# Kernel tuning notes

Hardware: AMD Instinct MI355X
Metric: run time of the kernel (lower is better)

## Reference

```python
import jax, jax.numpy as jnp
import numpy as np

N_HEADS, N_LEVELS, N_POINTS = 8, 4, 4
SPATIAL_SHAPES = np.array([[100, 100], [50, 50], [25, 25], [13, 13]], dtype=np.int32)


def setup_inputs() -> dict:
    key = jax.random.key(0)
    ks = jax.random.split(key, 6)
    N, Lq, C = 8, 4096, 256
    L_total = int(SPATIAL_SHAPES.prod(1).sum())  # 13294
    HLP = N_HEADS * N_LEVELS * N_POINTS  # 128
    return {
        "query": jax.random.normal(ks[0], (Lq, N, C), jnp.float32),
        "reference_points": jax.random.uniform(ks[1], (N, Lq, N_LEVELS, 2), jnp.float32),
        "feature_maps": jax.random.normal(ks[2], (L_total, N, C), jnp.float32),
        "spatial_shapes": SPATIAL_SHAPES,  # static numpy: drives reshapes
        "W_off": jax.random.normal(ks[3], (C, HLP * 2), jnp.float32) * 0.02,
        "b_off": jnp.zeros((HLP * 2,), jnp.float32),
        "W_attn": jax.random.normal(ks[4], (C, HLP), jnp.float32) * 0.02,
        "b_attn": jnp.zeros((HLP,), jnp.float32),
        "W_out": jax.random.normal(ks[5], (C, C), jnp.float32) / np.sqrt(C).astype(np.float32),
        "b_out": jnp.zeros((C,), jnp.float32),
    }


def bilinear_sample(img, gx, gy):
    """F.grid_sample(mode='bilinear', padding_mode='zeros', align_corners=False).
    img: (B, C, H, W); gx, gy: (B, P) normalized coords in [-1, 1]. -> (B, C, P)"""
    B, C, H, W = img.shape
    x = ((gx + 1.0) * W - 1.0) * 0.5
    y = ((gy + 1.0) * H - 1.0) * 0.5
    x0f = jnp.floor(x)
    y0f = jnp.floor(y)
    wx = x - x0f
    wy = y - y0f
    x0 = x0f.astype(jnp.int32)
    y0 = y0f.astype(jnp.int32)
    img_flat = img.reshape(B, C, H * W)

    def gather(ix, iy):
        valid = (ix >= 0) & (ix < W) & (iy >= 0) & (iy < H)
        idx = jnp.clip(iy, 0, H - 1) * W + jnp.clip(ix, 0, W - 1)  # (B, P)
        v = jax.vmap(lambda f, i: f[:, i])(img_flat, idx)  # (B, C, P)
        return v * valid[:, None, :].astype(img.dtype)

    v00 = gather(x0, y0)
    v01 = gather(x0 + 1, y0)
    v10 = gather(x0, y0 + 1)
    v11 = gather(x0 + 1, y0 + 1)
    w00 = ((1 - wx) * (1 - wy))[:, None, :]
    w01 = (wx * (1 - wy))[:, None, :]
    w10 = ((1 - wx) * wy)[:, None, :]
    w11 = (wx * wy)[:, None, :]
    return v00 * w00 + v01 * w01 + v10 * w10 + v11 * w11


def deform_attn(query, reference_points, feature_maps, spatial_shapes,
                W_off, b_off, W_attn, b_attn, W_out, b_out):
    Lq, N, C = query.shape
    H_, L_, P_ = N_HEADS, N_LEVELS, N_POINTS
    dh = C // H_
    q = jnp.transpose(query, (1, 0, 2))  # (N, Lq, C)
    off = (q @ W_off + b_off).reshape(N, Lq, H_, L_, P_, 2)
    attn = jax.nn.softmax((q @ W_attn + b_attn).reshape(N, Lq, H_, L_ * P_), axis=-1)
    attn = attn.reshape(N, Lq, H_, L_, P_)
    ss = np.asarray(spatial_shapes)  # (L, 2) as (H, W), static
    ss_flip = jnp.asarray(ss[:, ::-1].astype(np.float32))  # (L, 2) as (W, H)
    # sampling locations in [0,1], then to [-1,1] grid coords
    loc = reference_points[:, :, None, :, None, :] + off / ss_flip[None, None, None, :, None, :]
    grid = 2.0 * loc - 1.0  # (N, Lq, H, L, P, 2)
    starts = np.concatenate([[0], np.cumsum(ss.prod(1))[:-1]])
    sampled = []
    for lid in range(L_):
        Hl, Wl = int(ss[lid, 0]), int(ss[lid, 1])
        s = int(starts[lid])
        fm = feature_maps[s:s + Hl * Wl]  # (Hl*Wl, N, C)
        img = jnp.transpose(fm, (1, 2, 0)).reshape(N * H_, dh, Hl, Wl)
        g = jnp.transpose(grid[:, :, :, lid], (0, 2, 1, 3, 4)).reshape(N * H_, Lq * P_, 2)
        v = bilinear_sample(img, g[..., 0], g[..., 1])  # (N*H, dh, Lq*P)
        v = v.reshape(N, H_, dh, Lq, P_)
        sampled.append(jnp.transpose(v, (0, 3, 1, 2, 4)))  # (N, Lq, H, dh, P)
    sv = jnp.stack(sampled, axis=4)  # (N, Lq, H, dh, L, P)
    out = (attn[:, :, :, None, :, :] * sv).sum(axis=(-1, -2)).reshape(N, Lq, C)
    out = out @ W_out + b_out
    return jnp.transpose(out, (1, 0, 2))  # (Lq, N, C)


def reference(query, reference_points, feature_maps, spatial_shapes,
              W_off, b_off, W_attn, b_attn, W_out, b_out):
    return deform_attn(query, reference_points, feature_maps, spatial_shapes,
                       W_off, b_off, W_attn, b_attn, W_out, b_out)
```

## Files before the change

### kernel.cpp

```cpp
#include <hip/hip_runtime.h>

typedef unsigned short u16;
typedef __attribute__((ext_vector_type(8))) __bf16 bf16x8;
typedef __attribute__((ext_vector_type(4))) float f32x4;
typedef __attribute__((ext_vector_type(4))) int   i32x4;

#define NLQ 32768
#define WPN (384*256)
#define WON (256*256)
#define FMU 3403264

static __device__ __forceinline__ u16 f2bf(float f) {
    unsigned u = __float_as_uint(f);
    return (u16)((u + 0x7fffu + ((u >> 16) & 1u)) >> 16);
}
static __device__ __forceinline__ uint pk2(float lo, float hi) {
    return (uint)f2bf(lo) | ((uint)f2bf(hi) << 16);
}

__global__ __launch_bounds__(256) void wconv_kernel(
    const float* __restrict__ W_off, const float* __restrict__ W_attn,
    const float* __restrict__ W_out,
    u16* __restrict__ wtp, u16* __restrict__ wto)
{
    const int wi = blockIdx.x * 256 + threadIdx.x;
    if (wi < WPN) {
        int j = wi >> 8, k = wi & 255;
        float v = (j < 256) ? W_off[k * 256 + j] : W_attn[k * 128 + (j - 256)];
        wtp[wi] = f2bf(v);
    } else {
        int wi2 = wi - WPN;
        int j = wi2 >> 8, k = wi2 & 255;
        wto[wi2] = f2bf(W_out[k * 256 + j]);
    }
}

__global__ __launch_bounds__(256) void fmconv_kernel(
    const f32x4* __restrict__ fm, uint4* __restrict__ fmb)
{
    const int base = blockIdx.x * 2048 + threadIdx.x;
#pragma unroll
    for (int j = 0; j < 8; ++j) {
        int u = base + j * 256;
        if (u < FMU) {
            f32x4 lo = __builtin_nontemporal_load(fm + 2 * u);
            f32x4 hi = __builtin_nontemporal_load(fm + 2 * u + 1);
            uint4 r;
            r.x = pk2(lo.x, lo.y); r.y = pk2(lo.z, lo.w);
            r.z = pk2(hi.x, hi.y); r.w = pk2(hi.z, hi.w);
            fmb[u] = r;
        }
    }
}

__global__ __launch_bounds__(256) void proj_gemm(
    const float* __restrict__ query, const u16* __restrict__ Bt,
    const float* __restrict__ b_off, const float* __restrict__ b_attn,
    float* __restrict__ C)
{
    const int t = threadIdx.x;
    const int wid = t >> 6, lane = t & 63;
    const int lr = lane & 15, lk = lane >> 4;
    const int mrow = blockIdx.x * 128 + (wid >> 1) * 64;
    const int ncol = blockIdx.y * 128 + (wid & 1) * 64;
    const int kO = lk * 8;

    const float* qrow[4];
#pragma unroll
    for (int mi = 0; mi < 4; ++mi) {
        int gq = mrow + mi * 16 + lr;
        qrow[mi] = query + (size_t)((gq & 4095) * 8 + (gq >> 12)) * 256;
    }

    f32x4 acc[4][4] = {};
#pragma unroll
    for (int kk = 0; kk < 8; ++kk) {
        bf16x8 a[4], b[4];
#pragma unroll
        for (int mi = 0; mi < 4; ++mi) {
            f32x4 lo = *(const f32x4*)(qrow[mi] + kk * 32 + kO);
            f32x4 hi = *(const f32x4*)(qrow[mi] + kk * 32 + kO + 4);
#pragma unroll
            for (int j = 0; j < 4; ++j) {
                a[mi][j]     = (__bf16)lo[j];
                a[mi][4 + j] = (__bf16)hi[j];
            }
        }
#pragma unroll
        for (int ni = 0; ni < 4; ++ni)
            b[ni] = *(const bf16x8*)(Bt + (size_t)(ncol + ni * 16 + lr) * 256 + kk * 32 + kO);
#pragma unroll
        for (int mi = 0; mi < 4; ++mi)
#pragma unroll
            for (int ni = 0; ni < 4; ++ni)
                acc[mi][ni] = __builtin_amdgcn_mfma_f32_16x16x32_bf16(a[mi], b[ni], acc[mi][ni], 0, 0, 0);
    }

#pragma unroll
    for (int ni = 0; ni < 4; ++ni) {
        int gcol = ncol + ni * 16 + lr;
        float bias = (gcol < 256) ? b_off[gcol] : b_attn[gcol - 256];
#pragma unroll
        for (int mi = 0; mi < 4; ++mi) {
            f32x4 v = acc[mi][ni];
#pragma unroll
            for (int r = 0; r < 4; ++r)
                C[(size_t)(mrow + mi * 16 + lk * 4 + r) * 384 + gcol] = v[r] + bias;
        }
    }
}

__global__ __launch_bounds__(256) void sample_kernel(
    const u16* __restrict__ fmb,
    const float* __restrict__ proj,
    const float* __restrict__ refp,
    u16* __restrict__ mid)
{
    __shared__ i32x4 loff[256];
    __shared__ f32x4 lwv[256];
    const int t = threadIdx.x;
    const int ql = t >> 7, pt = t & 127;
    const int gq = blockIdx.x * 2 + ql;
    const int n = gq >> 12;

    {
        const int lp = pt & 15, l = lp >> 2;
        float lg = proj[(size_t)gq * 384 + 256 + pt];
        float m = lg;
#pragma unroll
        for (int msk = 1; msk < 16; msk <<= 1) m = fmaxf(m, __shfl_xor(m, msk));
        float e = __expf(lg - m);
        float s = e;
#pragma unroll
        for (int msk = 1; msk < 16; msk <<= 1) s += __shfl_xor(s, msk);
        float a = e / s;

        float ox = proj[(size_t)gq * 384 + 2 * pt];
        float oy = proj[(size_t)gq * 384 + 2 * pt + 1];
        int   Sl = (l == 0) ? 100 : (l == 1) ? 50 : (l == 2) ? 25 : 13;
        int   lb = (l == 0) ? 0 : (l == 1) ? 10000 : (l == 2) ? 12500 : 13125;
        float Sf = (float)Sl;
        float rx = refp[((size_t)gq * 4 + l) * 2 + 0];
        float ry = refp[((size_t)gq * 4 + l) * 2 + 1];
        float px = rx * Sf + ox - 0.5f;
        float py = ry * Sf + oy - 0.5f;
        float x0f = floorf(px), y0f = floorf(py);
        float wx = px - x0f, wy = py - y0f;
        int x0 = (int)x0f, y0 = (int)y0f;
        bool xv0 = (unsigned)x0 < (unsigned)Sl;
        bool xv1 = (unsigned)(x0 + 1) < (unsigned)Sl;
        bool yv0 = (unsigned)y0 < (unsigned)Sl;
        bool yv1 = (unsigned)(y0 + 1) < (unsigned)Sl;
        int x0c = min(max(x0, 0), Sl - 1), x1c = min(max(x0 + 1, 0), Sl - 1);
        int y0c = min(max(y0, 0), Sl - 1), y1c = min(max(y0 + 1, 0), Sl - 1);
        int r0 = (lb + y0c * Sl) << 12, r1 = (lb + y1c * Sl) << 12;
        i32x4 o; f32x4 w;
        o.x = r0 + (x0c << 12); o.y = r0 + (x1c << 12);
        o.z = r1 + (x0c << 12); o.w = r1 + (x1c << 12);
        w.x = (xv0 && yv0) ? a * (1.f - wx) * (1.f - wy) : 0.f;
        w.y = (xv1 && yv0) ? a * wx * (1.f - wy) : 0.f;
        w.z = (xv0 && yv1) ? a * (1.f - wx) * wy : 0.f;
        w.w = (xv1 && yv1) ? a * wx * wy : 0.f;
        loff[t] = o;
        lwv[t] = w;
    }
    __syncthreads();

    const int h = pt >> 4, ll = pt & 15, g2 = ll >> 2, cl = ll & 3;
    const uint boff = (uint)(n * 512 + h * 64 + cl * 16);
    const char* __restrict__ fb = (const char*)fmb;

    float a0 = 0.f, a1 = 0.f, a2 = 0.f, a3 = 0.f;
    float a4 = 0.f, a5 = 0.f, a6 = 0.f, a7 = 0.f;
#pragma unroll
    for (int pi = 0; pi < 4; ++pi) {
        int idx = ql * 128 + h * 16 + g2 * 4 + pi;
        i32x4 o = loff[idx];
        f32x4 w = lwv[idx];
        uint4 v0 = *(const uint4*)(fb + (boff + (uint)o.x));
        uint4 v1 = *(const uint4*)(fb + (boff + (uint)o.y));
        uint4 v2 = *(const uint4*)(fb + (boff + (uint)o.z));
        uint4 v3 = *(const uint4*)(fb + (boff + (uint)o.w));
#define ACC8(u, wt)                                        \
        a0 += wt * __uint_as_float(u.x << 16);             \
        a1 += wt * __uint_as_float(u.x & 0xFFFF0000u);     \
        a2 += wt * __uint_as_float(u.y << 16);             \
        a3 += wt * __uint_as_float(u.y & 0xFFFF0000u);     \
        a4 += wt * __uint_as_float(u.z << 16);             \
        a5 += wt * __uint_as_float(u.z & 0xFFFF0000u);     \
        a6 += wt * __uint_as_float(u.w << 16);             \
        a7 += wt * __uint_as_float(u.w & 0xFFFF0000u);
        ACC8(v0, w.x) ACC8(v1, w.y) ACC8(v2, w.z) ACC8(v3, w.w)
#undef ACC8
    }
#pragma unroll
    for (int msk = 4; msk <= 8; msk <<= 1) {
        a0 += __shfl_xor(a0, msk); a1 += __shfl_xor(a1, msk);
        a2 += __shfl_xor(a2, msk); a3 += __shfl_xor(a3, msk);
        a4 += __shfl_xor(a4, msk); a5 += __shfl_xor(a5, msk);
        a6 += __shfl_xor(a6, msk); a7 += __shfl_xor(a7, msk);
    }

    if (ll < 4) {
        uint4 r;
        r.x = pk2(a0, a1); r.y = pk2(a2, a3);
        r.z = pk2(a4, a5); r.w = pk2(a6, a7);
        ((uint4*)mid)[(size_t)gq * 32 + h * 4 + cl] = r;
    }
}

__global__ __launch_bounds__(256) void out_gemm(
    const u16* __restrict__ A, const u16* __restrict__ Bt,
    const float* __restrict__ b_out,
    float* __restrict__ out)
{
    const int t = threadIdx.x;
    const int wid = t >> 6, lane = t & 63;
    const int lr = lane & 15, lk = lane >> 4;
    const int mrow = blockIdx.x * 128 + (wid >> 1) * 64;
    const int ncol = blockIdx.y * 128 + (wid & 1) * 64;
    const int kO = lk * 8;

    f32x4 acc[4][4] = {};
#pragma unroll
    for (int kk = 0; kk < 8; ++kk) {
        bf16x8 a[4], b[4];
#pragma unroll
        for (int mi = 0; mi < 4; ++mi)
            a[mi] = *(const bf16x8*)(A + (size_t)(mrow + mi * 16 + lr) * 256 + kk * 32 + kO);
#pragma unroll
        for (int ni = 0; ni < 4; ++ni)
            b[ni] = *(const bf16x8*)(Bt + (size_t)(ncol + ni * 16 + lr) * 256 + kk * 32 + kO);
#pragma unroll
        for (int mi = 0; mi < 4; ++mi)
#pragma unroll
            for (int ni = 0; ni < 4; ++ni)
                acc[mi][ni] = __builtin_amdgcn_mfma_f32_16x16x32_bf16(a[mi], b[ni], acc[mi][ni], 0, 0, 0);
    }

#pragma unroll
    for (int ni = 0; ni < 4; ++ni) {
        int gcol = ncol + ni * 16 + lr;
        float bias = b_out[gcol];
#pragma unroll
        for (int mi = 0; mi < 4; ++mi) {
            f32x4 v = acc[mi][ni];
#pragma unroll
            for (int r = 0; r < 4; ++r) {
                int grow = mrow + mi * 16 + lk * 4 + r;
                int nn = grow >> 12, lq = grow & 4095;
                out[(size_t)(lq * 8 + nn) * 256 + gcol] = v[r] + bias;
            }
        }
    }
}

extern "C" void kernel_launch(void* const* d_in, const int* in_sizes, int n_in,
                              void* d_out, int out_size, void* d_ws, size_t ws_size,
                              hipStream_t stream) {
    const float* query  = (const float*)d_in[0];
    const float* refp   = (const float*)d_in[1];
    const float* fm     = (const float*)d_in[2];
    const float* W_off  = (const float*)d_in[4];
    const float* b_off  = (const float*)d_in[5];
    const float* W_attn = (const float*)d_in[6];
    const float* b_attn = (const float*)d_in[7];
    const float* W_out  = (const float*)d_in[8];
    const float* b_out  = (const float*)d_in[9];
    float* out = (float*)d_out;

    float* ws_proj = (float*)d_ws;
    u16*   wtp     = (u16*)(ws_proj + (size_t)NLQ * 384);
    u16*   wto     = wtp + (size_t)WPN;
    u16*   mid     = wto + (size_t)WON;
    u16*   fmb     = mid + (size_t)NLQ * 256;

    wconv_kernel<<<640, 256, 0, stream>>>(W_off, W_attn, W_out, wtp, wto);
    fmconv_kernel<<<1663, 256, 0, stream>>>((const f32x4*)fm, (uint4*)fmb);
    proj_gemm<<<dim3(256, 3), 256, 0, stream>>>(query, wtp, b_off, b_attn, ws_proj);
    sample_kernel<<<NLQ / 2, 256, 0, stream>>>(fmb, ws_proj, refp, mid);
    out_gemm<<<dim3(256, 2), 256, 0, stream>>>(mid, wto, b_out, out);
}
```

Before: 167.9 us.

## Switch pipeline to fp16, merge prep kernels, pre-convert query, use packed half FMA

```diff
diff --git a/kernel.cpp b/kernel.cpp
--- a/kernel.cpp
+++ b/kernel.cpp
@@ -1,7 +1,8 @@
 #include <hip/hip_runtime.h>
+#include <hip/hip_fp16.h>
 
 typedef unsigned short u16;
-typedef __attribute__((ext_vector_type(8))) __bf16 bf16x8;
+typedef __attribute__((ext_vector_type(8))) _Float16 f16x8;
 typedef __attribute__((ext_vector_type(4))) float f32x4;
 typedef __attribute__((ext_vector_type(4))) int   i32x4;
 
@@ -10,53 +11,78 @@
 #define WON (256*256)
 #define FMU 3403264
 
-static __device__ __forceinline__ u16 f2bf(float f) {
-    unsigned u = __float_as_uint(f);
-    return (u16)((u + 0x7fffu + ((u >> 16) & 1u)) >> 16);
-}
-static __device__ __forceinline__ uint pk2(float lo, float hi) {
-    return (uint)f2bf(lo) | ((uint)f2bf(hi) << 16);
-}
-
-__global__ __launch_bounds__(256) void wconv_kernel(
+static __device__ __forceinline__ uint pkh(float a, float b) {
+    __half2 h = __floats2half2_rn(a, b);
+    return *reinterpret_cast<uint*>(&h);
+}
+static __device__ __forceinline__ u16 f2h(float a) {
+    __half h = __float2half_rn(a);
+    return *reinterpret_cast<u16*>(&h);
+}
+static __device__ __forceinline__ __half2 bits2h2(uint u) {
+    return *reinterpret_cast<__half2*>(&u);
+}
+static __device__ __forceinline__ __half2 shfl_xor_h2(__half2 v, int m) {
+    int i = *reinterpret_cast<int*>(&v);
+    i = __shfl_xor(i, m);
+    return *reinterpret_cast<__half2*>(&i);
+}
+
+__global__ __launch_bounds__(256) void prep_kernel(
+    const f32x4* __restrict__ fm, uint4* __restrict__ fmb,
+    const float* __restrict__ query, uint4* __restrict__ qh4,
     const float* __restrict__ W_off, const float* __restrict__ W_attn,
     const float* __restrict__ W_out,
     u16* __restrict__ wtp, u16* __restrict__ wto)
 {
-    const int wi = blockIdx.x * 256 + threadIdx.x;
-    if (wi < WPN) {
-        int j = wi >> 8, k = wi & 255;
-        float v = (j < 256) ? W_off[k * 256 + j] : W_attn[k * 128 + (j - 256)];
-        wtp[wi] = f2bf(v);
+    const int b = blockIdx.x, t = threadIdx.x;
+    if (b < 1663) {
+        const int base = b * 2048 + t;
+#pragma unroll
+        for (int j = 0; j < 8; ++j) {
+            int u = base + j * 256;
+            if (u < FMU) {
+                f32x4 lo = __builtin_nontemporal_load(fm + 2 * u);
+                f32x4 hi = __builtin_nontemporal_load(fm + 2 * u + 1);
+                uint4 r;
+                r.x = pkh(lo.x, lo.y); r.y = pkh(lo.z, lo.w);
+                r.z = pkh(hi.x, hi.y); r.w = pkh(hi.z, hi.w);
+                fmb[u] = r;
+            }
+        }
+    } else if (b < 2175) {
+        const int base = (b - 1663) * 2048 + t;
+#pragma unroll
+        for (int j = 0; j < 8; ++j) {
+            int u = base + j * 256;
+            int gq = u >> 5, c = (u & 31) * 8;
+            int lq = gq & 4095, n = gq >> 12;
+            const f32x4* src = (const f32x4*)(query + ((size_t)(lq * 8 + n) << 8) + c);
+            f32x4 lo = __builtin_nontemporal_load(src);
+            f32x4 hi = __builtin_nontemporal_load(src + 1);
+            uint4 r;
+            r.x = pkh(lo.x, lo.y); r.y = pkh(lo.z, lo.w);
+            r.z = pkh(hi.x, hi.y); r.w = pkh(hi.z, hi.w);
+            qh4[u] = r;
+        }
     } else {
-        int wi2 = wi - WPN;
-        int j = wi2 >> 8, k = wi2 & 255;
-        wto[wi2] = f2bf(W_out[k * 256 + j]);
-    }
-}
-
-__global__ __launch_bounds__(256) void fmconv_kernel(
-    const f32x4* __restrict__ fm, uint4* __restrict__ fmb)
-{
-    const int base = blockIdx.x * 2048 + threadIdx.x;
-#pragma unroll
-    for (int j = 0; j < 8; ++j) {
-        int u = base + j * 256;
-        if (u < FMU) {
-            f32x4 lo = __builtin_nontemporal_load(fm + 2 * u);
-            f32x4 hi = __builtin_nontemporal_load(fm + 2 * u + 1);
-            uint4 r;
-            r.x = pk2(lo.x, lo.y); r.y = pk2(lo.z, lo.w);
-            r.z = pk2(hi.x, hi.y); r.w = pk2(hi.z, hi.w);
-            fmb[u] = r;
+        const int wi = (b - 2175) * 256 + t;
+        if (wi < WPN) {
+            int j = wi >> 8, k = wi & 255;
+            float v = (j < 256) ? W_off[k * 256 + j] : W_attn[k * 128 + (j - 256)];
+            wtp[wi] = f2h(v);
+        } else {
+            int wi2 = wi - WPN;
+            int j = wi2 >> 8, k = wi2 & 255;
+            wto[wi2] = f2h(W_out[k * 256 + j]);
         }
     }
 }
 
 __global__ __launch_bounds__(256) void proj_gemm(
-    const float* __restrict__ query, const u16* __restrict__ Bt,
+    const u16* __restrict__ A, const u16* __restrict__ Bt,
     const float* __restrict__ b_off, const float* __restrict__ b_attn,
-    float* __restrict__ C)
+    u16* __restrict__ C)
 {
     const int t = threadIdx.x;
     const int wid = t >> 6, lane = t & 63;
@@ -65,35 +91,21 @@
     const int ncol = blockIdx.y * 128 + (wid & 1) * 64;
     const int kO = lk * 8;
 
-    const float* qrow[4];
-#pragma unroll
-    for (int mi = 0; mi < 4; ++mi) {
-        int gq = mrow + mi * 16 + lr;
-        qrow[mi] = query + (size_t)((gq & 4095) * 8 + (gq >> 12)) * 256;
-    }
-
     f32x4 acc[4][4] = {};
 #pragma unroll
     for (int kk = 0; kk < 8; ++kk) {
-        bf16x8 a[4], b[4];
-#pragma unroll
-        for (int mi = 0; mi < 4; ++mi) {
-            f32x4 lo = *(const f32x4*)(qrow[mi] + kk * 32 + kO);
-            f32x4 hi = *(const f32x4*)(qrow[mi] + kk * 32 + kO + 4);
-#pragma unroll
-            for (int j = 0; j < 4; ++j) {
-                a[mi][j]     = (__bf16)lo[j];
-                a[mi][4 + j] = (__bf16)hi[j];
-            }
-        }
+        f16x8 a[4], b[4];
+#pragma unroll
+        for (int mi = 0; mi < 4; ++mi)
+            a[mi] = *(const f16x8*)(A + (size_t)(mrow + mi * 16 + lr) * 256 + kk * 32 + kO);
 #pragma unroll
         for (int ni = 0; ni < 4; ++ni)
-            b[ni] = *(const bf16x8*)(Bt + (size_t)(ncol + ni * 16 + lr) * 256 + kk * 32 + kO);
+            b[ni] = *(const f16x8*)(Bt + (size_t)(ncol + ni * 16 + lr) * 256 + kk * 32 + kO);
 #pragma unroll
         for (int mi = 0; mi < 4; ++mi)
 #pragma unroll
             for (int ni = 0; ni < 4; ++ni)
-                acc[mi][ni] = __builtin_amdgcn_mfma_f32_16x16x32_bf16(a[mi], b[ni], acc[mi][ni], 0, 0, 0);
+                acc[mi][ni] = __builtin_amdgcn_mfma_f32_16x16x32_f16(a[mi], b[ni], acc[mi][ni], 0, 0, 0);
     }
 
 #pragma unroll
@@ -105,19 +117,19 @@
             f32x4 v = acc[mi][ni];
 #pragma unroll
             for (int r = 0; r < 4; ++r)
-                C[(size_t)(mrow + mi * 16 + lk * 4 + r) * 384 + gcol] = v[r] + bias;
+                C[(size_t)(mrow + mi * 16 + lk * 4 + r) * 384 + gcol] = f2h(v[r] + bias);
         }
     }
 }
 
 __global__ __launch_bounds__(256) void sample_kernel(
     const u16* __restrict__ fmb,
-    const float* __restrict__ proj,
+    const u16* __restrict__ proj,
     const float* __restrict__ refp,
     u16* __restrict__ mid)
 {
     __shared__ i32x4 loff[256];
-    __shared__ f32x4 lwv[256];
+    __shared__ i32x4 lwp[256];
     const int t = threadIdx.x;
     const int ql = t >> 7, pt = t & 127;
     const int gq = blockIdx.x * 2 + ql;
@@ -125,7 +137,7 @@
 
     {
         const int lp = pt & 15, l = lp >> 2;
-        float lg = proj[(size_t)gq * 384 + 256 + pt];
+        float lg = __half2float(__ushort_as_half(proj[(size_t)gq * 384 + 256 + pt]));
         float m = lg;
 #pragma unroll
         for (int msk = 1; msk < 16; msk <<= 1) m = fmaxf(m, __shfl_xor(m, msk));
@@ -135,8 +147,8 @@
         for (int msk = 1; msk < 16; msk <<= 1) s += __shfl_xor(s, msk);
         float a = e / s;
 
-        float ox = proj[(size_t)gq * 384 + 2 * pt];
-        float oy = proj[(size_t)gq * 384 + 2 * pt + 1];
+        float ox = __half2float(__ushort_as_half(proj[(size_t)gq * 384 + 2 * pt]));
+        float oy = __half2float(__ushort_as_half(proj[(size_t)gq * 384 + 2 * pt + 1]));
         int   Sl = (l == 0) ? 100 : (l == 1) ? 50 : (l == 2) ? 25 : 13;
         int   lb = (l == 0) ? 0 : (l == 1) ? 10000 : (l == 2) ? 12500 : 13125;
         float Sf = (float)Sl;
@@ -154,15 +166,18 @@
         int x0c = min(max(x0, 0), Sl - 1), x1c = min(max(x0 + 1, 0), Sl - 1);
         int y0c = min(max(y0, 0), Sl - 1), y1c = min(max(y0 + 1, 0), Sl - 1);
         int r0 = (lb + y0c * Sl) << 12, r1 = (lb + y1c * Sl) << 12;
-        i32x4 o; f32x4 w;
+        i32x4 o;
         o.x = r0 + (x0c << 12); o.y = r0 + (x1c << 12);
         o.z = r1 + (x0c << 12); o.w = r1 + (x1c << 12);
-        w.x = (xv0 && yv0) ? a * (1.f - wx) * (1.f - wy) : 0.f;
-        w.y = (xv1 && yv0) ? a * wx * (1.f - wy) : 0.f;
-        w.z = (xv0 && yv1) ? a * (1.f - wx) * wy : 0.f;
-        w.w = (xv1 && yv1) ? a * wx * wy : 0.f;
+        float w0 = (xv0 && yv0) ? a * (1.f - wx) * (1.f - wy) : 0.f;
+        float w1 = (xv1 && yv0) ? a * wx * (1.f - wy) : 0.f;
+        float w2 = (xv0 && yv1) ? a * (1.f - wx) * wy : 0.f;
+        float w3 = (xv1 && yv1) ? a * wx * wy : 0.f;
+        i32x4 wp;
+        wp.x = (int)pkh(w0, w0); wp.y = (int)pkh(w1, w1);
+        wp.z = (int)pkh(w2, w2); wp.w = (int)pkh(w3, w3);
         loff[t] = o;
-        lwv[t] = w;
+        lwp[t] = wp;
     }
     __syncthreads();
 
@@ -170,41 +185,43 @@
     const uint boff = (uint)(n * 512 + h * 64 + cl * 16);
     const char* __restrict__ fb = (const char*)fmb;
 
-    float a0 = 0.f, a1 = 0.f, a2 = 0.f, a3 = 0.f;
-    float a4 = 0.f, a5 = 0.f, a6 = 0.f, a7 = 0.f;
+    __half2 z = __float2half2_rn(0.f);
+    __half2 a01 = z, a23 = z, a45 = z, a67 = z;
 #pragma unroll
     for (int pi = 0; pi < 4; ++pi) {
         int idx = ql * 128 + h * 16 + g2 * 4 + pi;
         i32x4 o = loff[idx];
-        f32x4 w = lwv[idx];
+        i32x4 wp = lwp[idx];
         uint4 v0 = *(const uint4*)(fb + (boff + (uint)o.x));
         uint4 v1 = *(const uint4*)(fb + (boff + (uint)o.y));
         uint4 v2 = *(const uint4*)(fb + (boff + (uint)o.z));
         uint4 v3 = *(const uint4*)(fb + (boff + (uint)o.w));
-#define ACC8(u, wt)                                        \
-        a0 += wt * __uint_as_float(u.x << 16);             \
-        a1 += wt * __uint_as_float(u.x & 0xFFFF0000u);     \
-        a2 += wt * __uint_as_float(u.y << 16);             \
-        a3 += wt * __uint_as_float(u.y & 0xFFFF0000u);     \
-        a4 += wt * __uint_as_float(u.z << 16);             \
-        a5 += wt * __uint_as_float(u.z & 0xFFFF0000u);     \
-        a6 += wt * __uint_as_float(u.w << 16);             \
-        a7 += wt * __uint_as_float(u.w & 0xFFFF0000u);
-        ACC8(v0, w.x) ACC8(v1, w.y) ACC8(v2, w.z) ACC8(v3, w.w)
-#undef ACC8
+        const uint4* vv[4] = {&v0, &v1, &v2, &v3};
+        const int    ww[4] = {wp.x, wp.y, wp.z, wp.w};
+#pragma unroll
+        for (int cn = 0; cn < 4; ++cn) {
+            __half2 wh = bits2h2((uint)ww[cn]);
+            uint4 vb = *vv[cn];
+            a01 = __hfma2(bits2h2(vb.x), wh, a01);
+            a23 = __hfma2(bits2h2(vb.y), wh, a23);
+            a45 = __hfma2(bits2h2(vb.z), wh, a45);
+            a67 = __hfma2(bits2h2(vb.w), wh, a67);
+        }
     }
 #pragma unroll
     for (int msk = 4; msk <= 8; msk <<= 1) {
-        a0 += __shfl_xor(a0, msk); a1 += __shfl_xor(a1, msk);
-        a2 += __shfl_xor(a2, msk); a3 += __shfl_xor(a3, msk);
-        a4 += __shfl_xor(a4, msk); a5 += __shfl_xor(a5, msk);
-        a6 += __shfl_xor(a6, msk); a7 += __shfl_xor(a7, msk);
+        a01 = __hadd2(a01, shfl_xor_h2(a01, msk));
+        a23 = __hadd2(a23, shfl_xor_h2(a23, msk));
+        a45 = __hadd2(a45, shfl_xor_h2(a45, msk));
+        a67 = __hadd2(a67, shfl_xor_h2(a67, msk));
     }
 
     if (ll < 4) {
         uint4 r;
-        r.x = pk2(a0, a1); r.y = pk2(a2, a3);
-        r.z = pk2(a4, a5); r.w = pk2(a6, a7);
+        r.x = *reinterpret_cast<uint*>(&a01);
+        r.y = *reinterpret_cast<uint*>(&a23);
+        r.z = *reinterpret_cast<uint*>(&a45);
+        r.w = *reinterpret_cast<uint*>(&a67);
         ((uint4*)mid)[(size_t)gq * 32 + h * 4 + cl] = r;
     }
 }
@@ -224,18 +241,18 @@
     f32x4 acc[4][4] = {};
 #pragma unroll
     for (int kk = 0; kk < 8; ++kk) {
-        bf16x8 a[4], b[4];
+        f16x8 a[4], b[4];
 #pragma unroll
         for (int mi = 0; mi < 4; ++mi)
-            a[mi] = *(const bf16x8*)(A + (size_t)(mrow + mi * 16 + lr) * 256 + kk * 32 + kO);
+            a[mi] = *(const f16x8*)(A + (size_t)(mrow + mi * 16 + lr) * 256 + kk * 32 + kO);
 #pragma unroll
         for (int ni = 0; ni < 4; ++ni)
-            b[ni] = *(const bf16x8*)(Bt + (size_t)(ncol + ni * 16 + lr) * 256 + kk * 32 + kO);
+            b[ni] = *(const f16x8*)(Bt + (size_t)(ncol + ni * 16 + lr) * 256 + kk * 32 + kO);
 #pragma unroll
         for (int mi = 0; mi < 4; ++mi)
 #pragma unroll
             for (int ni = 0; ni < 4; ++ni)
-                acc[mi][ni] = __builtin_amdgcn_mfma_f32_16x16x32_bf16(a[mi], b[ni], acc[mi][ni], 0, 0, 0);
+                acc[mi][ni] = __builtin_amdgcn_mfma_f32_16x16x32_f16(a[mi], b[ni], acc[mi][ni], 0, 0, 0);
     }
 
 #pragma unroll
@@ -269,15 +286,17 @@
     const float* b_out  = (const float*)d_in[9];
     float* out = (float*)d_out;
 
-    float* ws_proj = (float*)d_ws;
-    u16*   wtp     = (u16*)(ws_proj + (size_t)NLQ * 384);
-    u16*   wto     = wtp + (size_t)WPN;
-    u16*   mid     = wto + (size_t)WON;
-    u16*   fmb     = mid + (size_t)NLQ * 256;
-
-    wconv_kernel<<<640, 256, 0, stream>>>(W_off, W_attn, W_out, wtp, wto);
-    fmconv_kernel<<<1663, 256, 0, stream>>>((const f32x4*)fm, (uint4*)fmb);
-    proj_gemm<<<dim3(256, 3), 256, 0, stream>>>(query, wtp, b_off, b_attn, ws_proj);
+    u16* ws_proj = (u16*)d_ws;
+    u16* wtp     = ws_proj + (size_t)NLQ * 384;
+    u16* wto     = wtp + (size_t)WPN;
+    u16* mid     = wto + (size_t)WON;
+    u16* qh      = mid;
+    u16* fmb     = mid + (size_t)NLQ * 256;
+
+    prep_kernel<<<2815, 256, 0, stream>>>((const f32x4*)fm, (uint4*)fmb,
+                                          query, (uint4*)qh,
+                                          W_off, W_attn, W_out, wtp, wto);
+    proj_gemm<<<dim3(256, 3), 256, 0, stream>>>(qh, wtp, b_off, b_attn, ws_proj);
     sample_kernel<<<NLQ / 2, 256, 0, stream>>>(fmb, ws_proj, refp, mid);
     out_gemm<<<dim3(256, 2), 256, 0, stream>>>(mid, wto, b_out, out);
 }
```

New measurement: 155.1 us. 7.6% less time.
